# Optimization experiments

Hardware: AMD Instinct MI355X
Metric: run time of the kernel (lower is better)

The kernel has to match this reference:

```python
import jax, jax.numpy as jnp
import numpy as np

NUM_HEADS = 4
EPS = 1e-12  # torch F.normalize eps


def conv1x1(x, w):
    # x: (b,c,h,w), w: (co,ci,1,1) -> pointwise conv == channel GEMM
    return jnp.einsum('bchw,dc->bdhw', x, w[:, :, 0, 0])


def dwconv3x3(x, w):
    # depthwise 3x3, groups = channels; w: (c,1,3,3)
    c = x.shape[1]
    return jax.lax.conv_general_dilated(
        x, w, window_strides=(1, 1), padding=((1, 1), (1, 1)),
        dimension_numbers=('NCHW', 'OIHW', 'NCHW'), feature_group_count=c)


def l2_normalize(x, axis=-1):
    n = jnp.sqrt(jnp.sum(x * x, axis=axis, keepdims=True))
    return x / jnp.maximum(n, EPS)


def setup_inputs() -> dict:
    key = jax.random.key(0)
    ks = jax.random.split(key, 8)
    b, c, h, w = 4, 192, 128, 128
    s = 0.05
    return {
        'x': jax.random.normal(ks[0], (b, c, h, w), jnp.float32),
        'wq': jax.random.normal(ks[1], (c, c, 1, 1), jnp.float32) * s,
        'wq_dw': jax.random.normal(ks[2], (c, 1, 3, 3), jnp.float32) * s,
        'wk': jax.random.normal(ks[3], (c, c, 1, 1), jnp.float32) * s,
        'wk_dw': jax.random.normal(ks[4], (c, 1, 3, 3), jnp.float32) * s,
        'wv': jax.random.normal(ks[5], (c, c, 1, 1), jnp.float32) * s,
        'wv_dw': jax.random.normal(ks[6], (c, 1, 3, 3), jnp.float32) * s,
        'temperature': jnp.ones((NUM_HEADS, 1, 1), jnp.float32),
    }


def reference(x, wq, wq_dw, wk, wk_dw, wv, wv_dw, temperature):
    b, c, h, w = x.shape
    hd = NUM_HEADS
    ch = c // hd  # per-head channels
    n = h * w

    q = dwconv3x3(conv1x1(x, wq), wq_dw)
    k = dwconv3x3(conv1x1(x, wk), wk_dw)
    v = dwconv3x3(conv1x1(x, wv), wv_dw)

    # b (head c) h w -> b head c (h w)
    q = q.reshape(b, hd, ch, n)
    k = k.reshape(b, hd, ch, n)
    v = v.reshape(b, hd, ch, n)

    q = l2_normalize(q, axis=-1)
    k = l2_normalize(k, axis=-1)

    # channel-wise attention: (c x N) @ (N x c) -> (c x c)
    attn = jnp.einsum('bhcn,bhdn->bhcd', q, k) * temperature  # temperature: (head,1,1)
    attn = jax.nn.softmax(attn, axis=-1)
    out = jnp.einsum('bhcd,bhdn->bhcn', attn, v)
    return out.reshape(b, c, h, w)
```

## Files before the change

### kernel.cpp

```cpp
#include <hip/hip_runtime.h>
#include <hip/hip_bf16.h>


typedef __attribute__((ext_vector_type(8))) short short8;
typedef __attribute__((ext_vector_type(4))) float f32x4;

#define NB 4
#define NC 192
#define NN 16384
#define CH 48
#define NWELEM 115780
#define NZERO 38400

__device__ inline unsigned short f2bf(float f) {
  union { float f; unsigned int u; } c; c.f = f;
  unsigned int r = c.u + 0x7FFF + ((c.u >> 16) & 1);
  return (unsigned short)(r >> 16);
}
__device__ inline float bf2f(unsigned short u) {
  union { unsigned int u; float f; } c; c.u = ((unsigned int)u) << 16;
  return c.f;
}

__device__ inline bool detect_f32(const unsigned short* x) {
  int l = threadIdx.x & 63;
  unsigned short u = x[2 * (l * 997 + 1)];
  int e = (u >> 7) & 0xFF;
  bool extreme = (e < 90) || (e > 165);
  return __popcll(__ballot(extreme)) >= 8;
}

__global__ __launch_bounds__(256) void k_pre(const unsigned short* __restrict__ x,
                                             const void* wq, const void* wk, const void* wv,
                                             const void* wqd, const void* wkd, const void* wvd,
                                             const void* temp,
                                             unsigned short* __restrict__ canon,
                                             float* __restrict__ zbase) {
  int blk = blockIdx.x;
  if (blk >= 453) {
    int i = (blk - 453) * 256 + threadIdx.x;
    if (i < NZERO) zbase[i] = 0.f;
    return;
  }
  bool f32 = detect_f32(x);
  int i = blk * 256 + threadIdx.x;
  if (i >= NWELEM) return;
  const void* src; int off;
  if (i < 36864)       { src = wq;  off = i; }
  else if (i < 73728)  { src = wk;  off = i - 36864; }
  else if (i < 110592) { src = wv;  off = i - 73728; }
  else if (i < 112320) { src = wqd; off = i - 110592; }
  else if (i < 114048) { src = wkd; off = i - 112320; }
  else if (i < 115776) { src = wvd; off = i - 114048; }
  else                 { src = temp; off = i - 115776; }
  canon[i] = f32 ? f2bf(((const float*)src)[off])
                 : ((const unsigned short*)src)[off];
}

__global__ __launch_bounds__(256) void k_transpose(const unsigned short* __restrict__ X,
                                                   unsigned short* __restrict__ Xt) {
  __shared__ unsigned short tile[64 * 65];
  bool f32 = detect_f32(X);
  int b = blockIdx.z, c0 = blockIdx.y * 64, p0 = blockIdx.x * 64;
  int tid = threadIdx.x;
  if (f32) {
    const float* Xf = (const float*)X;
    for (int it = 0; it < 16; ++it) {
      int idx = it * 256 + tid;
      int c = idx >> 6, p = idx & 63;
      tile[c * 65 + p] = f2bf(Xf[((size_t)b * NC + c0 + c) * NN + p0 + p]);
    }
  } else {
    for (int it = 0; it < 16; ++it) {
      int idx = it * 256 + tid;
      int c = idx >> 6, p = idx & 63;
      tile[c * 65 + p] = X[((size_t)b * NC + c0 + c) * NN + p0 + p];
    }
  }
  __syncthreads();
  for (int it = 0; it < 2; ++it) {
    int idx = it * 256 + tid;
    int cc = idx & 7, p = idx >> 3;
    short8 v;
#pragma unroll
    for (int j = 0; j < 8; ++j) v[j] = (short)tile[(cc * 8 + j) * 65 + p];
    *(short8*)(Xt + ((size_t)b * NN + p0 + p) * NC + c0 + cc * 8) = v;
  }
}

#define LDP 200
__global__ __launch_bounds__(256) void k_conv(const unsigned short* __restrict__ Wall,
                                              const unsigned short* __restrict__ Xt,
                                              unsigned short* __restrict__ Yall) {
  __shared__ __align__(16) unsigned short Xs[64 * LDP];
  int b = blockIdx.y, p0 = blockIdx.x * 64;
  int tid = threadIdx.x;
  const unsigned short* tb = Xt + ((size_t)b * NN + p0) * NC;
  for (int it = 0; it < 6; ++it) {
    int idx = it * 256 + tid;
    short8 v = *(const short8*)(tb + idx * 8);
    int p = idx / 24, cc = idx % 24;
    *(short8*)(&Xs[p * LDP + cc * 8]) = v;
  }
  __syncthreads();
  int lane = tid & 63, w = tid >> 6;
  int lrow = lane & 15, lq = lane >> 4;
  short8 bf[6][4];
#pragma unroll
  for (int ks = 0; ks < 6; ++ks)
    for (int nt = 0; nt < 4; ++nt)
      bf[ks][nt] = *(const short8*)(&Xs[(nt * 16 + lrow) * LDP + ks * 32 + lq * 8]);
  short8 wreg[2][6];
#pragma unroll
  for (int ks = 0; ks < 6; ++ks)
    wreg[0][ks] = *(const short8*)(Wall + (size_t)(w * 16 + lrow) * NC + ks * 32 + lq * 8);
#pragma unroll
  for (int dt = 0; dt < 9; ++dt) {
    int cur = dt & 1, nxt = cur ^ 1;
    if (dt < 8) {
      int dR = (dt + 1) * 64 + w * 16 + lrow;
#pragma unroll
      for (int ks = 0; ks < 6; ++ks)
        wreg[nxt][ks] = *(const short8*)(Wall + (size_t)dR * NC + ks * 32 + lq * 8);
    }
    f32x4 acc[4];
#pragma unroll
    for (int nt = 0; nt < 4; ++nt) acc[nt] = (f32x4){0.f, 0.f, 0.f, 0.f};
#pragma unroll
    for (int ks = 0; ks < 6; ++ks)
      for (int nt = 0; nt < 4; ++nt)
        acc[nt] = __builtin_amdgcn_mfma_f32_16x16x32_bf16(bf[ks][nt], wreg[cur][ks], acc[nt], 0, 0, 0);
    int proj = dt / 3, c = (dt % 3) * 64 + w * 16 + lrow;
    unsigned short* Yb = Yall + (((size_t)proj * NB + b) * NC + c) * NN;
#pragma unroll
    for (int nt = 0; nt < 4; ++nt) {
      unsigned int u0 = ((unsigned int)f2bf(acc[nt][1]) << 16) | f2bf(acc[nt][0]);
      unsigned int u1 = ((unsigned int)f2bf(acc[nt][3]) << 16) | f2bf(acc[nt][2]);
      unsigned long long u = ((unsigned long long)u1 << 32) | u0;
      *(unsigned long long*)(Yb + p0 + nt * 16 + lq * 4) = u;
    }
  }
}

__device__ inline void cvtrow(short8 raw, unsigned short lo, unsigned short hi,
                              float* dst) {
  dst[0] = bf2f(lo);
#pragma unroll
  for (int j = 0; j < 8; ++j) dst[j + 1] = bf2f((unsigned short)raw[j]);
  dst[9] = bf2f(hi);
}

__global__ __launch_bounds__(256) void k_dwconv(const unsigned short* __restrict__ Yall,
                                                const unsigned short* __restrict__ Wdall,
                                                unsigned short* __restrict__ Pq,
                                                unsigned short* __restrict__ Pk,
                                                unsigned short* __restrict__ Pv,
                                                float* __restrict__ ssq,
                                                float* __restrict__ ssk) {
  int y = blockIdx.x, b = blockIdx.y;
  int proj = y / NC, c = y % NC;
  int tid = threadIdx.x;
  int lane = tid & 63, ch = tid & 15, rg = tid >> 4;
  const unsigned short* base = Yall + (((size_t)proj * NB + b) * NC + c) * NN;
  unsigned short* P = (proj == 0 ? Pq : (proj == 1 ? Pk : Pv));
  float* ss = (proj == 0 ? ssq : (proj == 1 ? ssk : nullptr));
  int r0 = rg * 8;

  short8 raw[10];
  unsigned short hl[10], hr[10];
#pragma unroll
  for (int i = 0; i < 10; ++i) {
    int gy = r0 - 1 + i;
    const unsigned short* rp = base + gy * 128 + ch * 8;
    if (gy >= 0 && gy < 128) {
      raw[i] = *(const short8*)rp;
      hl[i] = (ch > 0)  ? rp[-1] : (unsigned short)0;
      hr[i] = (ch < 15) ? rp[8]  : (unsigned short)0;
    } else {
      raw[i] = (short8){0, 0, 0, 0, 0, 0, 0, 0};
      hl[i] = 0;
      hr[i] = 0;
    }
  }

  float wk9[9];
#pragma unroll
  for (int i = 0; i < 9; ++i) wk9[i] = bf2f(Wdall[(proj * NC + c) * 9 + i]);

  float rows[3][10];
  cvtrow(raw[0], hl[0], hr[0], rows[0]);
  cvtrow(raw[1], hl[1], hr[1], rows[1]);
  float ssacc = 0.f;
#pragma unroll
  for (int r = 0; r < 8; ++r) {
    cvtrow(raw[r + 2], hl[r + 2], hr[r + 2], rows[(r + 2) % 3]);
    float z[8];
#pragma unroll
    for (int j = 0; j < 8; ++j) z[j] = 0.f;
#pragma unroll
    for (int dy = 0; dy < 3; ++dy) {
      const float* f = rows[(r + dy) % 3];
      float w0 = wk9[dy * 3], w1 = wk9[dy * 3 + 1], w2 = wk9[dy * 3 + 2];
#pragma unroll
      for (int j = 0; j < 8; ++j) z[j] += w0 * f[j] + w1 * f[j + 1] + w2 * f[j + 2];
    }
    short8 sv;
#pragma unroll
    for (int j = 0; j < 8; ++j) { sv[j] = (short)f2bf(z[j]); ssacc += z[j] * z[j]; }
    *(short8*)(P + ((size_t)b * NC + c) * NN + (r0 + r) * 128 + ch * 8) = sv;
  }
  if (ss) {
    for (int off = 32; off; off >>= 1) ssacc += __shfl_down(ssacc, off);
    if (lane == 0) atomicAdd(&ss[b * NC + c], ssacc);
  }
}

__global__ __launch_bounds__(256) void k_attn(const unsigned short* __restrict__ Qp,
                                              const unsigned short* __restrict__ Kp,
                                              float* __restrict__ S) {
  __shared__ float Sred[CH * CH];
  int bh = blockIdx.y, chunk = blockIdx.x;
  int b = bh >> 2, h = bh & 3;
  int tid = threadIdx.x, lane = tid & 63, w = tid >> 6;
  int lrow = lane & 15, lq = lane >> 4;
  const unsigned short* Qb = Qp + ((size_t)b * NC + h * CH) * NN;
  const unsigned short* Kb = Kp + ((size_t)b * NC + h * CH) * NN;
  int nbase = chunk * 1024 + w * 256;
  f32x4 acc[3][3];
  for (int i = 0; i < 3; ++i)
    for (int j = 0; j < 3; ++j) acc[i][j] = (f32x4){0.f, 0.f, 0.f, 0.f};
  for (int ks = 0; ks < 8; ++ks) {
    int n = nbase + ks * 32 + lq * 8;
    short8 a[3], bb[3];
    for (int t = 0; t < 3; ++t) a[t]  = *(const short8*)(Qb + (size_t)(t * 16 + lrow) * NN + n);
    for (int t = 0; t < 3; ++t) bb[t] = *(const short8*)(Kb + (size_t)(t * 16 + lrow) * NN + n);
    for (int ti = 0; ti < 3; ++ti)
      for (int tj = 0; tj < 3; ++tj)
        acc[ti][tj] = __builtin_amdgcn_mfma_f32_16x16x32_bf16(a[ti], bb[tj], acc[ti][tj], 0, 0, 0);
  }
  for (int i = tid; i < CH * CH; i += 256) Sred[i] = 0.f;
  __syncthreads();
  for (int ti = 0; ti < 3; ++ti)
    for (int tj = 0; tj < 3; ++tj)
      for (int r = 0; r < 4; ++r) {
        int row = ti * 16 + lq * 4 + r, col = tj * 16 + lrow;
        atomicAdd(&Sred[row * CH + col], acc[ti][tj][r]);
      }
  __syncthreads();
  float* Sg = S + bh * (CH * CH);
  for (int i = tid; i < CH * CH; i += 256) atomicAdd(&Sg[i], Sred[i]);
}

__global__ void k_softmax(const float* __restrict__ S, const float* __restrict__ ssq,
                          const float* __restrict__ ssk, const unsigned short* __restrict__ tempc,
                          float* __restrict__ AT) {
  int bh = blockIdx.x, b = bh >> 2, h = bh & 3;
  int i = threadIdx.x;
  if (i >= CH) return;
  float t = bf2f(tempc[h]);
  float rq = 1.f / fmaxf(sqrtf(ssq[b * NC + h * CH + i]), 1e-12f);
  const float* Srow = S + bh * (CH * CH) + i * CH;
  float l[CH];
  float m = -1e30f;
  for (int j = 0; j < CH; ++j) {
    float rk = 1.f / fmaxf(sqrtf(ssk[b * NC + h * CH + j]), 1e-12f);
    l[j] = Srow[j] * rq * rk * t;
    m = fmaxf(m, l[j]);
  }
  float s = 0.f;
  for (int j = 0; j < CH; ++j) { l[j] = __expf(l[j] - m); s += l[j]; }
  float inv = 1.f / s;
  for (int j = 0; j < CH; ++j) AT[bh * (CH * CH) + j * CH + i] = l[j] * inv;
}

__global__ __launch_bounds__(256) void k_out(const float* __restrict__ AT,
                                             const unsigned short* __restrict__ Vp,
                                             void* __restrict__ Out,
                                             const unsigned short* __restrict__ x) {
  bool f32 = detect_f32(x);
  int bh = blockIdx.y, b = bh >> 2, h = bh & 3;
  int p0 = (blockIdx.x * 256 + threadIdx.x) * 2;
  const float* A = AT + bh * (CH * CH);
  const unsigned short* Vb = Vp + ((size_t)b * NC + h * CH) * NN;
  float a1[CH], a2[CH];
  for (int i = 0; i < CH; ++i) { a1[i] = 0.f; a2[i] = 0.f; }
  for (int j = 0; j < CH; ++j) {
    unsigned int u = *(const unsigned int*)(Vb + (size_t)j * NN + p0);
    float v1 = bf2f((unsigned short)(u & 0xFFFF));
    float v2 = bf2f((unsigned short)(u >> 16));
    const float* Aj = A + j * CH;
    for (int i = 0; i < CH; ++i) {
      float a = Aj[i];
      a1[i] += a * v1;
      a2[i] += a * v2;
    }
  }
  size_t obase = ((size_t)b * NC + h * CH) * NN;
  if (f32) {
    float* Of = (float*)Out;
    for (int i = 0; i < CH; ++i)
      *(float2*)(Of + obase + (size_t)i * NN + p0) = make_float2(a1[i], a2[i]);
  } else {
    unsigned short* Ob = (unsigned short*)Out;
    for (int i = 0; i < CH; ++i) {
      unsigned int u = ((unsigned int)f2bf(a2[i]) << 16) | f2bf(a1[i]);
      *(unsigned int*)(Ob + obase + (size_t)i * NN + p0) = u;
    }
  }
}

extern "C" void kernel_launch(void* const* d_in, const int* in_sizes, int n_in,
                              void* d_out, int out_size, void* d_ws, size_t ws_size,
                              hipStream_t stream) {
  const unsigned short* x = (const unsigned short*)d_in[0];

  const size_t TEN = (size_t)NB * NC * NN;
  unsigned short* bufA = (unsigned short*)d_ws;
  unsigned short* bufB = bufA + TEN;
  unsigned short* bufV = bufB + TEN;
  unsigned short* Xt   = bufV + TEN;
  unsigned short* Yall = Xt + TEN;
  float* ssq = (float*)(Yall + 3 * TEN);
  float* ssk = ssq + NB * NC;
  float* S   = ssk + NB * NC;
  float* AT  = S + 16 * CH * CH;
  unsigned short* canon = (unsigned short*)(AT + 16 * CH * CH);
  const unsigned short* Wall = canon;
  const unsigned short* Wdall = canon + 110592;
  const unsigned short* Tmp = canon + 115776;

  k_pre<<<453 + (NZERO + 255) / 256, 256, 0, stream>>>(
      x, d_in[1], d_in[3], d_in[5], d_in[2], d_in[4], d_in[6], d_in[7], canon, ssq);
  k_transpose<<<dim3(NN / 64, NC / 64, NB), 256, 0, stream>>>(x, Xt);
  k_conv<<<dim3(NN / 64, NB), 256, 0, stream>>>(Wall, Xt, Yall);
  k_dwconv<<<dim3(3 * NC, NB), 256, 0, stream>>>(Yall, Wdall, bufA, bufB, bufV, ssq, ssk);
  k_attn<<<dim3(16, 16), 256, 0, stream>>>(bufA, bufB, S);
  k_softmax<<<16, 64, 0, stream>>>(S, ssq, ssk, Tmp, AT);
  k_out<<<dim3(NN / 512, 16), 256, 0, stream>>>(AT, bufV, d_out, x);
}
```

Measured before the change: 244.8 us.

## Fuse pointwise conv GEMM with depthwise 3x3 conv through shared memory

Merges the 1x1 conv GEMM and the depthwise 3x3 conv into one kernel. Each block computes a strip of 6 output rows plus halo rows for 32 output channels into LDS, then runs the depthwise stencil and sum-of-squares reduction from LDS. This removes the round trip of the three large intermediate projection tensors through global memory and one launch. In exchange it recomputes the halo rows (8 rows per 6 output rows), loads the weights per block, and adds an XCD-aware block index remap.

```diff
diff --git a/kernel.cpp b/kernel.cpp
--- a/kernel.cpp
+++ b/kernel.cpp
@@ -11,6 +11,7 @@
 #define CH 48
 #define NWELEM 115780
 #define NZERO 38400
+#define CST 1032
 
 __device__ inline unsigned short f2bf(float f) {
   union { float f; unsigned int u; } c; c.f = f;
@@ -88,130 +89,113 @@
   }
 }
 
-#define LDP 200
-__global__ __launch_bounds__(256) void k_conv(const unsigned short* __restrict__ Wall,
-                                              const unsigned short* __restrict__ Xt,
-                                              unsigned short* __restrict__ Yall) {
-  __shared__ __align__(16) unsigned short Xs[64 * LDP];
-  int b = blockIdx.y, p0 = blockIdx.x * 64;
-  int tid = threadIdx.x;
-  const unsigned short* tb = Xt + ((size_t)b * NN + p0) * NC;
-  for (int it = 0; it < 6; ++it) {
-    int idx = it * 256 + tid;
-    short8 v = *(const short8*)(tb + idx * 8);
-    int p = idx / 24, cc = idx % 24;
-    *(short8*)(&Xs[p * LDP + cc * 8]) = v;
-  }
-  __syncthreads();
-  int lane = tid & 63, w = tid >> 6;
-  int lrow = lane & 15, lq = lane >> 4;
-  short8 bf[6][4];
-#pragma unroll
-  for (int ks = 0; ks < 6; ++ks)
-    for (int nt = 0; nt < 4; ++nt)
-      bf[ks][nt] = *(const short8*)(&Xs[(nt * 16 + lrow) * LDP + ks * 32 + lq * 8]);
-  short8 wreg[2][6];
-#pragma unroll
-  for (int ks = 0; ks < 6; ++ks)
-    wreg[0][ks] = *(const short8*)(Wall + (size_t)(w * 16 + lrow) * NC + ks * 32 + lq * 8);
-#pragma unroll
-  for (int dt = 0; dt < 9; ++dt) {
-    int cur = dt & 1, nxt = cur ^ 1;
-    if (dt < 8) {
-      int dR = (dt + 1) * 64 + w * 16 + lrow;
-#pragma unroll
-      for (int ks = 0; ks < 6; ++ks)
-        wreg[nxt][ks] = *(const short8*)(Wall + (size_t)dR * NC + ks * 32 + lq * 8);
-    }
-    f32x4 acc[4];
-#pragma unroll
-    for (int nt = 0; nt < 4; ++nt) acc[nt] = (f32x4){0.f, 0.f, 0.f, 0.f};
-#pragma unroll
-    for (int ks = 0; ks < 6; ++ks)
-      for (int nt = 0; nt < 4; ++nt)
-        acc[nt] = __builtin_amdgcn_mfma_f32_16x16x32_bf16(bf[ks][nt], wreg[cur][ks], acc[nt], 0, 0, 0);
-    int proj = dt / 3, c = (dt % 3) * 64 + w * 16 + lrow;
-    unsigned short* Yb = Yall + (((size_t)proj * NB + b) * NC + c) * NN;
-#pragma unroll
-    for (int nt = 0; nt < 4; ++nt) {
-      unsigned int u0 = ((unsigned int)f2bf(acc[nt][1]) << 16) | f2bf(acc[nt][0]);
-      unsigned int u1 = ((unsigned int)f2bf(acc[nt][3]) << 16) | f2bf(acc[nt][2]);
-      unsigned long long u = ((unsigned long long)u1 << 32) | u0;
-      *(unsigned long long*)(Yb + p0 + nt * 16 + lq * 4) = u;
-    }
-  }
-}
-
-__device__ inline void cvtrow(short8 raw, unsigned short lo, unsigned short hi,
-                              float* dst) {
-  dst[0] = bf2f(lo);
-#pragma unroll
-  for (int j = 0; j < 8; ++j) dst[j + 1] = bf2f((unsigned short)raw[j]);
-  dst[9] = bf2f(hi);
-}
-
-__global__ __launch_bounds__(256) void k_dwconv(const unsigned short* __restrict__ Yall,
+__global__ __launch_bounds__(256) void k_convdw(const unsigned short* __restrict__ Wall,
+                                                const unsigned short* __restrict__ Xt,
                                                 const unsigned short* __restrict__ Wdall,
                                                 unsigned short* __restrict__ Pq,
                                                 unsigned short* __restrict__ Pk,
                                                 unsigned short* __restrict__ Pv,
                                                 float* __restrict__ ssq,
                                                 float* __restrict__ ssk) {
-  int y = blockIdx.x, b = blockIdx.y;
-  int proj = y / NC, c = y % NC;
-  int tid = threadIdx.x;
-  int lane = tid & 63, ch = tid & 15, rg = tid >> 4;
-  const unsigned short* base = Yall + (((size_t)proj * NB + b) * NC + c) * NN;
+  __shared__ __align__(16) unsigned short Y[32 * CST];
+  int gx = blockIdx.x, b = blockIdx.y;
+  int xcd = gx & 7, slot = gx >> 3;
+  int L = (xcd < 4) ? xcd * 50 + slot : 200 + (xcd - 4) * 49 + slot;
+  int dchunk = L % 18, strip = L / 18;
+  int r0 = strip * 6;
+  int tid = threadIdx.x, lane = tid & 63, w = tid >> 6;
+  int lrow = lane & 15, lq = lane >> 4;
+
+  const unsigned short* Wb = Wall + (size_t)(dchunk * 32) * NC;
+  short8 wreg[2][6];
+#pragma unroll
+  for (int df = 0; df < 2; ++df)
+#pragma unroll
+    for (int ks = 0; ks < 6; ++ks)
+      wreg[df][ks] = *(const short8*)(Wb + (size_t)(df * 16 + lrow) * NC + ks * 32 + lq * 8);
+#pragma unroll
+  for (int i = 0; i < 16; ++i) {
+    int pf = w * 16 + i;
+    int lr = pf >> 3;
+    int pxl = (pf & 7) * 16;
+    int gr = r0 - 1 + lr;
+    int yoff = lr * 128 + pxl + lq * 4;
+    if (gr >= 0 && gr < 128) {
+      const unsigned short* ap = Xt + ((size_t)b * NN + gr * 128 + pxl + lrow) * NC;
+      short8 a[6];
+#pragma unroll
+      for (int ks = 0; ks < 6; ++ks) a[ks] = *(const short8*)(ap + ks * 32 + lq * 8);
+#pragma unroll
+      for (int df = 0; df < 2; ++df) {
+        f32x4 acc = (f32x4){0.f, 0.f, 0.f, 0.f};
+#pragma unroll
+        for (int ks = 0; ks < 6; ++ks)
+          acc = __builtin_amdgcn_mfma_f32_16x16x32_bf16(a[ks], wreg[df][ks], acc, 0, 0, 0);
+        unsigned int u0 = ((unsigned int)f2bf(acc[1]) << 16) | f2bf(acc[0]);
+        unsigned int u1 = ((unsigned int)f2bf(acc[3]) << 16) | f2bf(acc[2]);
+        unsigned long long u = ((unsigned long long)u1 << 32) | u0;
+        *(unsigned long long*)(&Y[(df * 16 + lrow) * CST + yoff]) = u;
+      }
+    } else {
+#pragma unroll
+      for (int df = 0; df < 2; ++df)
+        *(unsigned long long*)(&Y[(df * 16 + lrow) * CST + yoff]) = 0ULL;
+    }
+  }
+  __syncthreads();
+
+  int proj = dchunk / 6;
+  int cbase = (dchunk % 6) * 32;
   unsigned short* P = (proj == 0 ? Pq : (proj == 1 ? Pk : Pv));
   float* ss = (proj == 0 ? ssq : (proj == 1 ? ssk : nullptr));
-  int r0 = rg * 8;
-
-  short8 raw[10];
-  unsigned short hl[10], hr[10];
-#pragma unroll
-  for (int i = 0; i < 10; ++i) {
-    int gy = r0 - 1 + i;
-    const unsigned short* rp = base + gy * 128 + ch * 8;
-    if (gy >= 0 && gy < 128) {
-      raw[i] = *(const short8*)rp;
-      hl[i] = (ch > 0)  ? rp[-1] : (unsigned short)0;
-      hr[i] = (ch < 15) ? rp[8]  : (unsigned short)0;
-    } else {
-      raw[i] = (short8){0, 0, 0, 0, 0, 0, 0, 0};
-      hl[i] = 0;
-      hr[i] = 0;
-    }
-  }
-
-  float wk9[9];
-#pragma unroll
-  for (int i = 0; i < 9; ++i) wk9[i] = bf2f(Wdall[(proj * NC + c) * 9 + i]);
-
-  float rows[3][10];
-  cvtrow(raw[0], hl[0], hr[0], rows[0]);
-  cvtrow(raw[1], hl[1], hr[1], rows[1]);
-  float ssacc = 0.f;
-#pragma unroll
-  for (int r = 0; r < 8; ++r) {
-    cvtrow(raw[r + 2], hl[r + 2], hr[r + 2], rows[(r + 2) % 3]);
-    float z[8];
-#pragma unroll
-    for (int j = 0; j < 8; ++j) z[j] = 0.f;
-#pragma unroll
-    for (int dy = 0; dy < 3; ++dy) {
-      const float* f = rows[(r + dy) % 3];
-      float w0 = wk9[dy * 3], w1 = wk9[dy * 3 + 1], w2 = wk9[dy * 3 + 2];
-#pragma unroll
-      for (int j = 0; j < 8; ++j) z[j] += w0 * f[j] + w1 * f[j + 1] + w2 * f[j + 2];
-    }
-    short8 sv;
-#pragma unroll
-    for (int j = 0; j < 8; ++j) { sv[j] = (short)f2bf(z[j]); ssacc += z[j] * z[j]; }
-    *(short8*)(P + ((size_t)b * NC + c) * NN + (r0 + r) * 128 + ch * 8) = sv;
-  }
-  if (ss) {
-    for (int off = 32; off; off >>= 1) ssacc += __shfl_down(ssacc, off);
-    if (lane == 0) atomicAdd(&ss[b * NC + c], ssacc);
+  int chunk = tid & 15, cidx = tid >> 4;
+#pragma unroll
+  for (int cpass = 0; cpass < 2; ++cpass) {
+    int cl = cidx + cpass * 16;
+    int cg = cbase + cl;
+    float wk9[9];
+#pragma unroll
+    for (int i = 0; i < 9; ++i) wk9[i] = bf2f(Wdall[(proj * NC + cg) * 9 + i]);
+    const unsigned short* yb = &Y[cl * CST];
+    float rows_[3][10];
+#define LOADL(sr, dst) {                                                   \
+      short8 v = *(const short8*)(yb + (sr) * 128 + chunk * 8);            \
+      (dst)[0] = (chunk > 0) ? bf2f(yb[(sr) * 128 + chunk * 8 - 1]) : 0.f; \
+      _Pragma("unroll")                                                    \
+      for (int j = 0; j < 8; ++j) (dst)[j + 1] = bf2f((unsigned short)v[j]); \
+      (dst)[9] = (chunk < 15) ? bf2f(yb[(sr) * 128 + chunk * 8 + 8]) : 0.f; }
+    LOADL(0, rows_[0]);
+    LOADL(1, rows_[1]);
+    float ssacc = 0.f;
+#pragma unroll
+    for (int rr = 0; rr < 6; ++rr) {
+      LOADL(rr + 2, rows_[(rr + 2) % 3]);
+      int r = r0 + rr;
+      float z[8];
+#pragma unroll
+      for (int j = 0; j < 8; ++j) z[j] = 0.f;
+#pragma unroll
+      for (int dy = 0; dy < 3; ++dy) {
+        const float* f = rows_[(rr + dy) % 3];
+        float w0 = wk9[dy * 3], w1 = wk9[dy * 3 + 1], w2 = wk9[dy * 3 + 2];
+#pragma unroll
+        for (int j = 0; j < 8; ++j) z[j] += w0 * f[j] + w1 * f[j + 1] + w2 * f[j + 2];
+      }
+      if (r < 128) {
+        short8 sv;
+#pragma unroll
+        for (int j = 0; j < 8; ++j) { sv[j] = (short)f2bf(z[j]); ssacc += z[j] * z[j]; }
+        *(short8*)(P + ((size_t)b * NC + cg) * NN + r * 128 + chunk * 8) = sv;
+      }
+    }
+#undef LOADL
+    if (ss) {
+      ssacc += __shfl_down(ssacc, 8);
+      ssacc += __shfl_down(ssacc, 4);
+      ssacc += __shfl_down(ssacc, 2);
+      ssacc += __shfl_down(ssacc, 1);
+      if ((lane & 15) == 0) atomicAdd(&ss[b * NC + cg], ssacc);
+    }
   }
 }
 
@@ -319,8 +303,7 @@
   unsigned short* bufB = bufA + TEN;
   unsigned short* bufV = bufB + TEN;
   unsigned short* Xt   = bufV + TEN;
-  unsigned short* Yall = Xt + TEN;
-  float* ssq = (float*)(Yall + 3 * TEN);
+  float* ssq = (float*)(Xt + TEN);
   float* ssk = ssq + NB * NC;
   float* S   = ssk + NB * NC;
   float* AT  = S + 16 * CH * CH;
@@ -332,8 +315,7 @@
   k_pre<<<453 + (NZERO + 255) / 256, 256, 0, stream>>>(
       x, d_in[1], d_in[3], d_in[5], d_in[2], d_in[4], d_in[6], d_in[7], canon, ssq);
   k_transpose<<<dim3(NN / 64, NC / 64, NB), 256, 0, stream>>>(x, Xt);
-  k_conv<<<dim3(NN / 64, NB), 256, 0, stream>>>(Wall, Xt, Yall);
-  k_dwconv<<<dim3(3 * NC, NB), 256, 0, stream>>>(Yall, Wdall, bufA, bufB, bufV, ssq, ssk);
+  k_convdw<<<dim3(396, NB), 256, 0, stream>>>(Wall, Xt, Wdall, bufA, bufB, bufV, ssq, ssk);
   k_attn<<<dim3(16, 16), 256, 0, stream>>>(bufA, bufB, S);
   k_softmax<<<16, 64, 0, stream>>>(S, ssq, ssk, Tmp, AT);
   k_out<<<dim3(NN / 512, 16), 256, 0, stream>>>(AT, bufV, d_out, x);
```

Measured after the change: 272.6 us. 11.4% more time.
